# Optimization experiments

Measured on AMD Instinct MI355X. Metric: run time of the kernel, lower is better.

## Reference

```python
import jax, jax.numpy as jnp
import numpy as np

B, W, S, D, H = 16, 128, 16, 768, 12
HD = D // H

def _ln(x, g, b):
    m = x.mean(-1, keepdims=True)
    v = ((x - m) ** 2).mean(-1, keepdims=True)
    return (x - m) / jnp.sqrt(v + 1e-5) * g + b

def _lin(x, w, b):
    return x @ w.T + b

def _rope(t):
    # t: (N, H, L, HD); interleaved even/odd rotation, base 10000
    inv = 1.0 / (10000.0 ** (jnp.arange(0, HD, 2, dtype=jnp.float32) / HD))
    fr = jnp.arange(t.shape[2], dtype=jnp.float32)[:, None] * inv[None, :]  # (L, HD//2)
    cos, sin = jnp.cos(fr), jnp.sin(fr)
    te, to = t[..., ::2], t[..., 1::2]
    return jnp.stack([te * cos - to * sin, te * sin + to * cos], -1).reshape(t.shape)

def _mha(q, k, v, mask=None):
    # q,k,v: (N, H, L, HD)
    s = jnp.einsum('nhqd,nhkd->nhqk', q, k) / jnp.sqrt(jnp.float32(HD))
    if mask is not None:
        s = jnp.where(mask[None, None], -jnp.inf, s)
    a = jax.nn.softmax(s, axis=-1)
    return jnp.einsum('nhqk,nhkd->nhqd', a, v)

def _heads(t, L):
    return t.reshape(-1, L, H, HD).transpose(0, 2, 1, 3)

def setup_inputs() -> dict:
    key = jax.random.key(0)
    ks = jax.random.split(key, 16)
    def w(i, shape):
        return jax.random.normal(ks[i], shape, jnp.float32) * 0.02
    return {
        'x': jax.random.normal(ks[0], (B, W, S, D), jnp.float32),
        'causal_mask': jnp.triu(jnp.ones((W, W), dtype=bool), k=1),
        'sn_g': jnp.ones((D,), jnp.float32), 'sn_b': jnp.zeros((D,), jnp.float32),
        'sa_in_w': w(1, (3 * D, D)), 'sa_in_b': jnp.zeros((3 * D,), jnp.float32),
        'sa_out_w': w(2, (D, D)), 'sa_out_b': jnp.zeros((D,), jnp.float32),
        'tn_g': jnp.ones((D,), jnp.float32), 'tn_b': jnp.zeros((D,), jnp.float32),
        'tq_w': w(3, (D, D)), 'tq_b': jnp.zeros((D,), jnp.float32),
        'tk_w': w(4, (D, D)), 'tk_b': jnp.zeros((D,), jnp.float32),
        'tv_w': w(5, (D, D)), 'tv_b': jnp.zeros((D,), jnp.float32),
        'to_w': w(6, (D, D)), 'to_b': jnp.zeros((D,), jnp.float32),
        'fn_g': jnp.ones((D,), jnp.float32), 'fn_b': jnp.zeros((D,), jnp.float32),
        'f1_w': w(7, (4 * D, D)), 'f1_b': jnp.zeros((4 * D,), jnp.float32),
        'f2_w': w(8, (D, 4 * D)), 'f2_b': jnp.zeros((D,), jnp.float32),
    }

def reference(x, causal_mask, sn_g, sn_b, sa_in_w, sa_in_b, sa_out_w, sa_out_b,
              tn_g, tn_b, tq_w, tq_b, tk_w, tk_b, tv_w, tv_b, to_w, to_b,
              fn_g, fn_b, f1_w, f1_b, f2_w, f2_b):
    # ---- spatial attention within each timestep: (B*W, S, D) ----
    xs = x.reshape(B * W, S, D)
    xn = _ln(xs, sn_g, sn_b)
    q, k, v = jnp.split(_lin(xn, sa_in_w, sa_in_b), 3, axis=-1)
    o = _mha(_heads(q, S), _heads(k, S), _heads(v, S))
    o = o.transpose(0, 2, 1, 3).reshape(B * W, S, D)
    xs = xs + _lin(o, sa_out_w, sa_out_b)
    x = xs.reshape(B, W, S, D)
    # ---- causal temporal attention with RoPE: (B*S, W, D) ----
    xt = x.transpose(0, 2, 1, 3).reshape(B * S, W, D)
    xn = _ln(xt, tn_g, tn_b)
    q = _rope(_heads(_lin(xn, tq_w, tq_b), W))
    k = _rope(_heads(_lin(xn, tk_w, tk_b), W))
    v = _heads(_lin(xn, tv_w, tv_b), W)
    o = _mha(q, k, v, causal_mask)
    o = o.transpose(0, 2, 1, 3).reshape(B * S, W, D)
    xt = xt + _lin(o, to_w, to_b)
    x = xt.reshape(B, S, W, D).transpose(0, 2, 1, 3)
    # ---- feed-forward (exact GELU, as torch default) ----
    h = jax.nn.gelu(_lin(_ln(x, fn_g, fn_b), f1_w, f1_b), approximate=False)
    return x + _lin(h, f2_w, f2_b)
```

## Files before the change

kernel.cpp:

```cpp
#include <hip/hip_runtime.h>
#include <stdint.h>


#define NB 16
#define NW 128
#define NS 16
#define ND 768
#define NH 12
#define NTOK 32768

typedef __attribute__((ext_vector_type(8))) short short8;
typedef __attribute__((ext_vector_type(4))) float f32x4;

__device__ __forceinline__ float blo(unsigned v){ return __builtin_bit_cast(float, v << 16); }
__device__ __forceinline__ float bhi(unsigned v){ return __builtin_bit_cast(float, v & 0xffff0000u); }
__device__ __forceinline__ float bus(unsigned short u){ return __builtin_bit_cast(float, ((unsigned)u) << 16); }
__device__ __forceinline__ unsigned short f2b(float f){
  unsigned u = __builtin_bit_cast(unsigned, f);
  u += 0x7fffu + ((u >> 16) & 1u);
  return (unsigned short)(u >> 16);
}
__device__ __forceinline__ void gld_lds16(const void* g, void* l){
  __builtin_amdgcn_global_load_lds((const __attribute__((address_space(1))) void*)g,
                                   (__attribute__((address_space(3))) void*)l, 16, 0, 0);
}

__global__ __launch_bounds__(256) void convert_k(const float* __restrict__ in,
                                                 unsigned short* __restrict__ out, int n4){
  int i = blockIdx.x * 256 + threadIdx.x;
  int stride = gridDim.x * 256;
  for (; i < n4; i += stride){
    float4 v = ((const float4*)in)[i];
    unsigned lo = (unsigned)f2b(v.x) | ((unsigned)f2b(v.y) << 16);
    unsigned hi = (unsigned)f2b(v.z) | ((unsigned)f2b(v.w) << 16);
    ((uint2*)out)[i] = make_uint2(lo, hi);
  }
}

__global__ __launch_bounds__(256) void concat3_k(const float* __restrict__ a, const float* __restrict__ b,
                                                 const float* __restrict__ c, float* __restrict__ o){
  int i = blockIdx.x * 256 + threadIdx.x;
  if (i < 768){ o[i] = a[i]; o[768 + i] = b[i]; o[1536 + i] = c[i]; }
}

__global__ __launch_bounds__(256) void rope_k(float* __restrict__ tab){
  int i = blockIdx.x * 256 + threadIdx.x;
  if (i < 128 * 32){
    int w = i >> 5, p = i & 31;
    float inv = powf(10000.0f, -((float)(2 * p)) / 64.0f);
    float ang = (float)w * inv;
    tab[i * 2] = cosf(ang);
    tab[i * 2 + 1] = sinf(ang);
  }
}

template<int INF32>
__global__ __launch_bounds__(256) void ln_k(const void* __restrict__ xin, const float* __restrict__ g,
                                            const float* __restrict__ bt, unsigned short* __restrict__ out){
  const int row = blockIdx.x;
  const int t = threadIdx.x;
  const float* xf = (const float*)xin;
  const unsigned short* xb = (const unsigned short*)xin;
  float v[3];
#pragma unroll
  for (int i = 0; i < 3; ++i){
    int j = t + i * 256;
    v[i] = INF32 ? xf[(size_t)row * 768 + j] : bus(xb[(size_t)row * 768 + j]);
  }
  float s = v[0] + v[1] + v[2];
  float ss = v[0]*v[0] + v[1]*v[1] + v[2]*v[2];
#pragma unroll
  for (int o = 1; o < 64; o <<= 1){ s += __shfl_xor(s, o, 64); ss += __shfl_xor(ss, o, 64); }
  __shared__ float red[8];
  int w = t >> 6;
  if ((t & 63) == 0){ red[w*2] = s; red[w*2+1] = ss; }
  __syncthreads();
  s = red[0] + red[2] + red[4] + red[6];
  ss = red[1] + red[3] + red[5] + red[7];
  float mean = s * (1.0f / 768.0f);
  float var = ss * (1.0f / 768.0f) - mean * mean;
  float rstd = rsqrtf(var + 1e-5f);
#pragma unroll
  for (int i = 0; i < 3; ++i){
    int j = t + i * 256;
    out[(size_t)row * 768 + j] = f2b((v[i] - mean) * rstd * g[j] + bt[j]);
  }
}

template<int MODE, int MROWS>
__global__ __launch_bounds__(512) void gemm256_k(const unsigned short* __restrict__ A,
                                                 const unsigned short* __restrict__ Bw,
                                                 const float* __restrict__ bias,
                                                 const void* __restrict__ resid,
                                                 void* __restrict__ outp, int K, int M){
  constexpr int MH = MROWS / 2;
  constexpr int ASH = (MROWS == 8) ? 14 : 13;
  constexpr int NJA = MROWS / 4;
  constexpr int LDSZ = 4 * (1 << ASH) + 65536;
  __shared__ char LB[LDSZ];
  char* const Asl = LB;
  char* const Bsl = LB + 4 * (1 << ASH);
  const int tid = threadIdx.x;
  const int lane = tid & 63, w = tid >> 6;
  const int llo = lane & 15, lhi = lane >> 4;
  const int wm = w >> 2, wn = w & 3;
  const int NT = K >> 6;

  const int gx = gridDim.x;
  const int nwg = gx * gridDim.y;
  const int orig = blockIdx.y * gx + blockIdx.x;
  const int lin = (nwg & 7) ? orig : ((orig & 7) * (nwg >> 3) + (orig >> 3));
  const int by = lin / gx, bx = lin - by * gx;
  const int brow = by * (MROWS << 5);
  const int bcol = bx << 8;

  const int r0 = tid >> 3, cp = tid & 7;
  const int swz = (cp << 4) ^ ((r0 & 7) << 4);
  const char* aG = (const char*)(A + (size_t)(brow + r0) * K) + swz;
  const char* bG = (const char*)(Bw + (size_t)(bcol + r0) * K) + swz;
  const int J  = K * 128;
  const int Ha = K * (MROWS << 5);
  const int Hb = K * 256;
  const int ldst = w << 10;

  auto stage_a = [&](int gb, char* slotbase){
    gld_lds16(aG + gb, slotbase + ldst);
    if constexpr (NJA == 2) gld_lds16(aG + gb + J, slotbase + ldst + (1 << 13));
  };
  auto stage_b = [&](int gb, char* slotbase){
    gld_lds16(bG + gb, slotbase + ldst);
    gld_lds16(bG + gb + J, slotbase + ldst + (1 << 13));
  };

  short8 a0[MH][2], a1[MH][2], b0[2][2], b1[2][2];
  auto rd_a = [&](short8 (&dst)[MH][2], const char* Ab, int rbase){
#pragma unroll
    for (int mi = 0; mi < MH; ++mi){
      const int rr = rbase + (mi << 4) + llo;
#pragma unroll
      for (int ks = 0; ks < 2; ++ks)
        dst[mi][ks] = *(const short8*)(Ab + rr * 128 + (((ks << 6) + (lhi << 4)) ^ ((rr & 7) << 4)));
    }
  };
  auto rd_b = [&](short8 (&dst)[2][2], const char* Bb, int cbase){
#pragma unroll
    for (int ni = 0; ni < 2; ++ni){
      const int cc = cbase + (ni << 4) + llo;
#pragma unroll
      for (int ks = 0; ks < 2; ++ks)
        dst[ni][ks] = *(const short8*)(Bb + cc * 128 + (((ks << 6) + (lhi << 4)) ^ ((cc & 7) << 4)));
    }
  };

  f32x4 acc[MROWS][4];
#pragma unroll
  for (int m = 0; m < MROWS; ++m)
#pragma unroll
    for (int n = 0; n < 4; ++n) acc[m][n] = f32x4{0.f, 0.f, 0.f, 0.f};

  auto mfma_q = [&](int mo, int no, short8 (&bb)[2][2], short8 (&aa)[MH][2]){
    __builtin_amdgcn_s_setprio(1);
#pragma unroll
    for (int mi = 0; mi < MH; ++mi)
#pragma unroll
      for (int ni = 0; ni < 2; ++ni){
        acc[mo + mi][no + ni] = __builtin_amdgcn_mfma_f32_16x16x32_bf16(bb[ni][0], aa[mi][0], acc[mo + mi][no + ni], 0, 0, 0);
        acc[mo + mi][no + ni] = __builtin_amdgcn_mfma_f32_16x16x32_bf16(bb[ni][1], aa[mi][1], acc[mo + mi][no + ni], 0, 0, 0);
      }
    __builtin_amdgcn_s_setprio(0);
  };

  stage_a(0,        Asl);
  stage_a(Ha,       Asl + (1 << ASH));
  stage_b(0,        Bsl);
  stage_b(Hb,       Bsl + (1 << 14));
  stage_a(128,      Asl + (2 << ASH));
  stage_a(128 + Ha, Asl + (3 << ASH));
  if constexpr (NJA == 2) asm volatile("s_waitcnt vmcnt(4)" ::: "memory");
  else                    asm volatile("s_waitcnt vmcnt(2)" ::: "memory");
  __builtin_amdgcn_s_barrier();
  {
    const char* Ab0 = Asl + ((wm & 3) << ASH);
    const char* Bb0 = Bsl + (((wn >> 1) & 3) << 14);
    rd_b(b0, Bb0, (wn & 1) << 6);
    rd_a(a0, Ab0, 0);
  }

  for (int t = 0; t < NT; ++t){
    const char* Ab = Asl + (((2 * t + wm) & 3) << ASH);
    const char* Bb = Bsl + (((2 * t + (wn >> 1)) & 3) << 14);
    const int tb = t << 7;

    rd_a(a1, Ab, MH << 4);
    __builtin_amdgcn_s_barrier();
    mfma_q(0, 0, b0, a0);
    __builtin_amdgcn_s_barrier();

    rd_b(b1, Bb, ((wn & 1) << 6) + 32);
    if (t + 1 < NT) stage_b(tb + 128, Bsl + (((2 * t + 2) & 3) << 14));
    __builtin_amdgcn_s_barrier();
    mfma_q(MH, 0, b0, a1);
    __builtin_amdgcn_s_barrier();

    if (t + 1 < NT) stage_b(tb + 128 + Hb, Bsl + (((2 * t + 3) & 3) << 14));
    if (t + 2 < NT) stage_a(tb + 256, Asl + (((2 * t + 4) & 3) << ASH));
    __builtin_amdgcn_s_barrier();
    mfma_q(0, 2, b1, a0);
    __builtin_amdgcn_s_barrier();

    if (t + 2 < NT){
      stage_a(tb + 256 + Ha, Asl + (((2 * t + 5) & 3) << ASH));
      if constexpr (NJA == 2) asm volatile("s_waitcnt vmcnt(4)" ::: "memory");
      else                    asm volatile("s_waitcnt vmcnt(2)" ::: "memory");
    } else {
      asm volatile("s_waitcnt vmcnt(0)" ::: "memory");
    }
    __builtin_amdgcn_s_barrier();
    if (t + 1 < NT){
      const char* Abn = Asl + (((2 * t + 2 + wm) & 3) << ASH);
      const char* Bbn = Bsl + (((2 * t + 2 + (wn >> 1)) & 3) << 14);
      rd_b(b0, Bbn, (wn & 1) << 6);
      rd_a(a0, Abn, 0);
    }
    mfma_q(MH, 2, b1, a1);
    __builtin_amdgcn_s_barrier();
  }

  const int orow = brow + wm * (MROWS << 4);
  const int ocol = bcol + (wn << 6);
  const unsigned short* resb = (const unsigned short*)resid;
  const float* resf = (const float*)resid;
#pragma unroll
  for (int m = 0; m < MROWS; ++m){
    const int row = orow + (m << 4) + llo;
    const size_t rb = (size_t)row * M;
#pragma unroll
    for (int n = 0; n < 4; ++n){
      const int col = ocol + (n << 4) + (lhi << 2);
      const float4 bv = *(const float4*)&bias[col];
      float v0 = acc[m][n][0] + bv.x;
      float v1 = acc[m][n][1] + bv.y;
      float v2 = acc[m][n][2] + bv.z;
      float v3 = acc[m][n][3] + bv.w;
      const size_t off = rb + col;
      if (MODE == 1){
        float y0 = v0 * (1.5957691216f + 0.0713548163f * v0 * v0);
        float y1 = v1 * (1.5957691216f + 0.0713548163f * v1 * v1);
        float y2 = v2 * (1.5957691216f + 0.0713548163f * v2 * v2);
        float y3 = v3 * (1.5957691216f + 0.0713548163f * v3 * v3);
        v0 = v0 / (1.0f + __expf(-y0));
        v1 = v1 / (1.0f + __expf(-y1));
        v2 = v2 / (1.0f + __expf(-y2));
        v3 = v3 / (1.0f + __expf(-y3));
      } else if (MODE == 2){
        const float4 rv = *(const float4*)&resf[off];
        v0 += rv.x; v1 += rv.y; v2 += rv.z; v3 += rv.w;
      } else if (MODE == 3 || MODE == 4){
        const uint2 rv = *(const uint2*)&resb[off];
        v0 += blo(rv.x); v1 += bhi(rv.x); v2 += blo(rv.y); v3 += bhi(rv.y);
      }
      if (MODE == 4){
        float4 ov; ov.x = v0; ov.y = v1; ov.z = v2; ov.w = v3;
        *(float4*)&((float*)outp)[off] = ov;
      } else {
        unsigned lo = (unsigned)f2b(v0) | ((unsigned)f2b(v1) << 16);
        unsigned hi = (unsigned)f2b(v2) | ((unsigned)f2b(v3) << 16);
        *(uint2*)&((unsigned short*)outp)[off] = make_uint2(lo, hi);
      }
    }
  }
}

__global__ __launch_bounds__(256) void sattn_k(const unsigned short* __restrict__ qkv,
                                               unsigned short* __restrict__ o){
  const int bw = blockIdx.x, h = blockIdx.y;
  const int t = threadIdx.x;
  __shared__ unsigned short qh[16 * 68], kh[16 * 68], vh[16 * 68];
  __shared__ float pl[16 * 17];
  const int row = t >> 4, c4 = t & 15;
  const size_t base = ((size_t)(bw * 16 + row)) * 2304 + h * 64 + c4 * 4;
  *(uint2*)&qh[row * 68 + c4 * 4] = *(const uint2*)&qkv[base];
  *(uint2*)&kh[row * 68 + c4 * 4] = *(const uint2*)&qkv[base + 768];
  *(uint2*)&vh[row * 68 + c4 * 4] = *(const uint2*)&qkv[base + 1536];
  __syncthreads();

  const int q = row, k = c4;
  float s = 0.f;
#pragma unroll
  for (int c = 0; c < 16; ++c){
    uint2 qv = *(const uint2*)&qh[q * 68 + c * 4];
    uint2 kv = *(const uint2*)&kh[k * 68 + c * 4];
    s += blo(qv.x) * blo(kv.x) + bhi(qv.x) * bhi(kv.x);
    s += blo(qv.y) * blo(kv.y) + bhi(qv.y) * bhi(kv.y);
  }
  s *= 0.125f;
  float m = s;
#pragma unroll
  for (int off = 1; off < 16; off <<= 1) m = fmaxf(m, __shfl_xor(m, off, 64));
  float p = __expf(s - m);
  float su = p;
#pragma unroll
  for (int off = 1; off < 16; off <<= 1) su += __shfl_xor(su, off, 64);
  pl[q * 17 + k] = p / su;
  __syncthreads();

  float o0 = 0.f, o1 = 0.f, o2 = 0.f, o3 = 0.f;
#pragma unroll
  for (int kk = 0; kk < 16; ++kk){
    float pw = pl[q * 17 + kk];
    uint2 vv = *(const uint2*)&vh[kk * 68 + c4 * 4];
    o0 += pw * blo(vv.x); o1 += pw * bhi(vv.x);
    o2 += pw * blo(vv.y); o3 += pw * bhi(vv.y);
  }
  const size_t ob = ((size_t)(bw * 16 + q)) * 768 + h * 64 + c4 * 4;
  unsigned r0 = (unsigned)f2b(o0) | ((unsigned)f2b(o1) << 16);
  unsigned r1 = (unsigned)f2b(o2) | ((unsigned)f2b(o3) << 16);
  *(uint2*)&o[ob] = make_uint2(r0, r1);
}

__global__ __launch_bounds__(256) void tattn_k(const unsigned short* __restrict__ qkv,
                                               const float* __restrict__ rope,
                                               unsigned short* __restrict__ o){
  const int bs = blockIdx.x, h = blockIdx.y;
  const int b = bs >> 4, s = bs & 15;
  const int t = threadIdx.x, lane = t & 63, w = t >> 6;
  const int lhi = lane >> 4, llo = lane & 15;
  __shared__ unsigned short Qs[128 * 64];
  __shared__ unsigned short Ks[128 * 64];
  __shared__ unsigned short Vt[64 * 128];
  __shared__ unsigned short P[128 * 128];

  {
    const int r = t >> 1;
    const int dbase = (t & 1) * 32;
    const size_t tokb = ((size_t)((b * 128 + r) * 16 + s)) * 2304 + h * 64;
    const float2* rp = (const float2*)rope;
#pragma unroll
    for (int mch = 0; mch < 4; ++mch){
      const int d0 = dbase + mch * 8;
      uint4 qv = *(const uint4*)&qkv[tokb + d0];
      uint4 kv = *(const uint4*)&qkv[tokb + 768 + d0];
      uint4 vv = *(const uint4*)&qkv[tokb + 1536 + d0];
      unsigned qin[4] = {qv.x, qv.y, qv.z, qv.w};
      unsigned kin[4] = {kv.x, kv.y, kv.z, kv.w};
      unsigned qo[4], ko[4];
#pragma unroll
      for (int j = 0; j < 4; ++j){
        float2 cssn = rp[r * 32 + (d0 >> 1) + j];
        float cs = cssn.x, sn = cssn.y;
        float qe = blo(qin[j]), qd = bhi(qin[j]);
        float ke = blo(kin[j]), kd = bhi(kin[j]);
        qo[j] = (unsigned)f2b(qe * cs - qd * sn) | ((unsigned)f2b(qe * sn + qd * cs) << 16);
        ko[j] = (unsigned)f2b(ke * cs - kd * sn) | ((unsigned)f2b(ke * sn + kd * cs) << 16);
      }
      const int byq = r * 128 + ((d0 * 2) ^ ((r & 7) << 4));
      *(uint4*)((char*)Qs + byq) = make_uint4(qo[0], qo[1], qo[2], qo[3]);
      *(uint4*)((char*)Ks + byq) = make_uint4(ko[0], ko[1], ko[2], ko[3]);
      unsigned vin[4] = {vv.x, vv.y, vv.z, vv.w};
#pragma unroll
      for (int j = 0; j < 8; ++j){
        const int d = d0 + j;
        unsigned short val = (j & 1) ? (unsigned short)(vin[j >> 1] >> 16)
                                     : (unsigned short)(vin[j >> 1] & 0xffffu);
        *(unsigned short*)((char*)Vt + d * 256 + ((r * 2) ^ ((d & 7) << 4))) = val;
      }
    }
  }
  __syncthreads();

  const int qbase = w * 32;
  f32x4 st[8][2];
#pragma unroll
  for (int i = 0; i < 8; ++i){ st[i][0] = f32x4{0.f,0.f,0.f,0.f}; st[i][1] = f32x4{0.f,0.f,0.f,0.f}; }
#pragma unroll
  for (int kd = 0; kd < 2; ++kd){
    short8 bq[2];
#pragma unroll
    for (int fq = 0; fq < 2; ++fq){
      const int qr = qbase + fq * 16 + llo;
      bq[fq] = *(const short8*)((const char*)Qs + qr * 128 + ((kd * 64 + lhi * 16) ^ ((qr & 7) << 4)));
    }
#pragma unroll
    for (int fk = 0; fk < 8; ++fk){
      const int kr = fk * 16 + llo;
      short8 ak = *(const short8*)((const char*)Ks + kr * 128 + ((kd * 64 + lhi * 16) ^ ((kr & 7) << 4)));
      st[fk][0] = __builtin_amdgcn_mfma_f32_16x16x32_bf16(ak, bq[0], st[fk][0], 0, 0, 0);
      st[fk][1] = __builtin_amdgcn_mfma_f32_16x16x32_bf16(ak, bq[1], st[fk][1], 0, 0, 0);
    }
  }

#pragma unroll
  for (int fq = 0; fq < 2; ++fq){
    const int qg = qbase + fq * 16 + llo;
    float m = -1e30f;
#pragma unroll
    for (int fk = 0; fk < 8; ++fk)
#pragma unroll
      for (int rr = 0; rr < 4; ++rr){
        const int kg = fk * 16 + lhi * 4 + rr;
        float sv = (kg <= qg) ? st[fk][fq][rr] : -1e30f;
        st[fk][fq][rr] = sv;
        m = fmaxf(m, sv);
      }
    m = fmaxf(m, __shfl_xor(m, 16, 64));
    m = fmaxf(m, __shfl_xor(m, 32, 64));
    float su = 0.f;
#pragma unroll
    for (int fk = 0; fk < 8; ++fk)
#pragma unroll
      for (int rr = 0; rr < 4; ++rr){
        float p = __expf((st[fk][fq][rr] - m) * 0.125f);
        st[fk][fq][rr] = p;
        su += p;
      }
    su += __shfl_xor(su, 16, 64);
    su += __shfl_xor(su, 32, 64);
    const float rs = 1.0f / su;
#pragma unroll
    for (int fk = 0; fk < 8; ++fk){
      const int kk = fk * 16 + lhi * 4;
      unsigned lo = (unsigned)f2b(st[fk][fq][0] * rs) | ((unsigned)f2b(st[fk][fq][1] * rs) << 16);
      unsigned hi = (unsigned)f2b(st[fk][fq][2] * rs) | ((unsigned)f2b(st[fk][fq][3] * rs) << 16);
      *(uint2*)((char*)P + qg * 256 + ((kk * 2) ^ ((qg & 7) << 4))) = make_uint2(lo, hi);
    }
  }
  __syncthreads();

  f32x4 oacc[2][4];
#pragma unroll
  for (int i = 0; i < 2; ++i)
#pragma unroll
    for (int j = 0; j < 4; ++j) oacc[i][j] = f32x4{0.f,0.f,0.f,0.f};
#pragma unroll
  for (int ks = 0; ks < 4; ++ks){
    short8 pa[2];
#pragma unroll
    for (int fq = 0; fq < 2; ++fq){
      const int qr = qbase + fq * 16 + llo;
      pa[fq] = *(const short8*)((const char*)P + qr * 256 + ((ks * 64 + lhi * 16) ^ ((qr & 7) << 4)));
    }
#pragma unroll
    for (int fd = 0; fd < 4; ++fd){
      const int dr = fd * 16 + llo;
      short8 vb = *(const short8*)((const char*)Vt + dr * 256 + ((ks * 64 + lhi * 16) ^ ((dr & 7) << 4)));
      oacc[0][fd] = __builtin_amdgcn_mfma_f32_16x16x32_bf16(pa[0], vb, oacc[0][fd], 0, 0, 0);
      oacc[1][fd] = __builtin_amdgcn_mfma_f32_16x16x32_bf16(pa[1], vb, oacc[1][fd], 0, 0, 0);
    }
  }

#pragma unroll
  for (int fq = 0; fq < 2; ++fq)
#pragma unroll
    for (int fd = 0; fd < 4; ++fd)
#pragma unroll
      for (int rr = 0; rr < 4; ++rr){
        const int qg = qbase + fq * 16 + lhi * 4 + rr;
        const int d = fd * 16 + llo;
        const size_t ob = ((size_t)((b * 128 + qg) * 16 + s)) * 768 + h * 64 + d;
        o[ob] = f2b(oacc[fq][fd][rr]);
      }
}

__global__ __launch_bounds__(256) void sentinel_k(float* out){
  if (blockIdx.x == 0 && threadIdx.x == 0) out[0] = 12345.0f;
}

extern "C" void kernel_launch(void* const* d_in, const int* in_sizes, int n_in,
                              void* d_out, int out_size, void* d_ws, size_t ws_size,
                              hipStream_t stream){
  const float* x       = (const float*)d_in[0];
  const float* sn_g    = (const float*)d_in[2];
  const float* sn_b    = (const float*)d_in[3];
  const float* sa_in_w = (const float*)d_in[4];
  const float* sa_in_b = (const float*)d_in[5];
  const float* sa_out_w= (const float*)d_in[6];
  const float* sa_out_b= (const float*)d_in[7];
  const float* tn_g    = (const float*)d_in[8];
  const float* tn_b    = (const float*)d_in[9];
  const float* tq_w    = (const float*)d_in[10];
  const float* tq_b    = (const float*)d_in[11];
  const float* tk_w    = (const float*)d_in[12];
  const float* tk_b    = (const float*)d_in[13];
  const float* tv_w    = (const float*)d_in[14];
  const float* tv_b    = (const float*)d_in[15];
  const float* to_w    = (const float*)d_in[16];
  const float* to_b    = (const float*)d_in[17];
  const float* fn_g    = (const float*)d_in[18];
  const float* fn_b    = (const float*)d_in[19];
  const float* f1_w    = (const float*)d_in[20];
  const float* f1_b    = (const float*)d_in[21];
  const float* f2_w    = (const float*)d_in[22];
  const float* f2_b    = (const float*)d_in[23];

  char* ws = (char*)d_ws;
  size_t off = 0;
  auto alloc = [&](size_t bytes) -> void* {
    void* p = ws + off;
    off += (bytes + 255) & ~(size_t)255;
    return p;
  };
  unsigned short* Wqkv = (unsigned short*)alloc((size_t)2304*768*2);
  unsigned short* Wo1  = (unsigned short*)alloc((size_t)768*768*2);
  unsigned short* W3   = (unsigned short*)alloc((size_t)2304*768*2);
  float*          b3   = (float*)alloc(2304*4);
  unsigned short* Wto  = (unsigned short*)alloc((size_t)768*768*2);
  unsigned short* Wf1  = (unsigned short*)alloc((size_t)3072*768*2);
  unsigned short* Wf2  = (unsigned short*)alloc((size_t)768*3072*2);
  float*          rope = (float*)alloc(128*32*2*4);
  unsigned short* xn   = (unsigned short*)alloc((size_t)NTOK*768*2);
  unsigned short* qkv  = (unsigned short*)alloc((size_t)NTOK*3072*2);
  unsigned short* xs2  = (unsigned short*)alloc((size_t)NTOK*768*2);
  unsigned short* xt2  = (unsigned short*)alloc((size_t)NTOK*768*2);
  unsigned short* ob   = xn;

  if (ws_size < off){ sentinel_k<<<1, 64, 0, stream>>>((float*)d_out); return; }

  convert_k<<<1024, 256, 0, stream>>>(sa_in_w, Wqkv, 2304*768/4);
  convert_k<<<512, 256, 0, stream>>>(sa_out_w, Wo1, 768*768/4);
  convert_k<<<512, 256, 0, stream>>>(tq_w, W3, 768*768/4);
  convert_k<<<512, 256, 0, stream>>>(tk_w, W3 + 768*768, 768*768/4);
  convert_k<<<512, 256, 0, stream>>>(tv_w, W3 + 2*768*768, 768*768/4);
  concat3_k<<<3, 256, 0, stream>>>(tq_b, tk_b, tv_b, b3);
  convert_k<<<512, 256, 0, stream>>>(to_w, Wto, 768*768/4);
  convert_k<<<1024, 256, 0, stream>>>(f1_w, Wf1, 3072*768/4);
  convert_k<<<1024, 256, 0, stream>>>(f2_w, Wf2, 768*3072/4);
  rope_k<<<16, 256, 0, stream>>>(rope);

  ln_k<1><<<NTOK, 256, 0, stream>>>(x, sn_g, sn_b, xn);
  gemm256_k<0,4><<<dim3(9, 256), 512, 0, stream>>>(xn, Wqkv, sa_in_b, nullptr, qkv, 768, 2304);
  sattn_k<<<dim3(2048, 12), 256, 0, stream>>>(qkv, ob);
  gemm256_k<2,4><<<dim3(3, 256), 512, 0, stream>>>(ob, Wo1, sa_out_b, x, xs2, 768, 768);

  ln_k<0><<<NTOK, 256, 0, stream>>>(xs2, tn_g, tn_b, xn);
  gemm256_k<0,4><<<dim3(9, 256), 512, 0, stream>>>(xn, W3, b3, nullptr, qkv, 768, 2304);
  tattn_k<<<dim3(256, 12), 256, 0, stream>>>(qkv, rope, ob);
  gemm256_k<3,4><<<dim3(3, 256), 512, 0, stream>>>(ob, Wto, to_b, xs2, xt2, 768, 768);

  ln_k<0><<<NTOK, 256, 0, stream>>>(xt2, fn_g, fn_b, xn);
  gemm256_k<1,8><<<dim3(12, 128), 512, 0, stream>>>(xn, Wf1, f1_b, nullptr, qkv, 768, 3072);
  gemm256_k<4,4><<<dim3(3, 256), 512, 0, stream>>>(qkv, Wf2, f2_b, xt2, d_out, 3072, 768);
}
```

Baseline: 1.176 ms.

## Replace 256-wide 8-wave GEMM with 128x128 4-wave tile at two blocks per CU

The large 512-thread GEMM, with a 128x256 or 256x256 output tile and 96-128KB of LDS, is replaced by a 256-thread kernel that computes a 128x128 tile and uses 64KB of LDS. Its launch bounds request two blocks per CU. The software pipeline is restructured: fragments are now read from LDS at each quarter-step, guarded by explicit lgkmcnt waits, instead of being prefetched across the barrier. The aim is higher occupancy and more blocks for load balance, at the cost of lower arithmetic intensity per tile, more global/L2 traffic, and more exposed LDS latency.

```diff
diff --git a/kernel.cpp b/kernel.cpp
--- a/kernel.cpp
+++ b/kernel.cpp
@@ -87,23 +87,19 @@
   }
 }
 
-template<int MODE, int MROWS>
-__global__ __launch_bounds__(512) void gemm256_k(const unsigned short* __restrict__ A,
-                                                 const unsigned short* __restrict__ Bw,
-                                                 const float* __restrict__ bias,
-                                                 const void* __restrict__ resid,
-                                                 void* __restrict__ outp, int K, int M){
-  constexpr int MH = MROWS / 2;
-  constexpr int ASH = (MROWS == 8) ? 14 : 13;
-  constexpr int NJA = MROWS / 4;
-  constexpr int LDSZ = 4 * (1 << ASH) + 65536;
-  __shared__ char LB[LDSZ];
+template<int MODE>
+__global__ __launch_bounds__(256, 2) void gemm128_k(const unsigned short* __restrict__ A,
+                                                    const unsigned short* __restrict__ Bw,
+                                                    const float* __restrict__ bias,
+                                                    const void* __restrict__ resid,
+                                                    void* __restrict__ outp, int K, int M){
+  __shared__ char LB[65536];
   char* const Asl = LB;
-  char* const Bsl = LB + 4 * (1 << ASH);
+  char* const Bsl = LB + 32768;
   const int tid = threadIdx.x;
   const int lane = tid & 63, w = tid >> 6;
   const int llo = lane & 15, lhi = lane >> 4;
-  const int wm = w >> 2, wn = w & 3;
+  const int wm = w >> 1, wn = w & 1;
   const int NT = K >> 6;
 
   const int gx = gridDim.x;
@@ -111,31 +107,26 @@
   const int orig = blockIdx.y * gx + blockIdx.x;
   const int lin = (nwg & 7) ? orig : ((orig & 7) * (nwg >> 3) + (orig >> 3));
   const int by = lin / gx, bx = lin - by * gx;
-  const int brow = by * (MROWS << 5);
-  const int bcol = bx << 8;
+  const int brow = by << 7;
+  const int bcol = bx << 7;
 
   const int r0 = tid >> 3, cp = tid & 7;
   const int swz = (cp << 4) ^ ((r0 & 7) << 4);
   const char* aG = (const char*)(A + (size_t)(brow + r0) * K) + swz;
   const char* bG = (const char*)(Bw + (size_t)(bcol + r0) * K) + swz;
-  const int J  = K * 128;
-  const int Ha = K * (MROWS << 5);
-  const int Hb = K * 256;
+  const int J  = K * 64;
+  const int Hh = K * 128;
   const int ldst = w << 10;
 
-  auto stage_a = [&](int gb, char* slotbase){
-    gld_lds16(aG + gb, slotbase + ldst);
-    if constexpr (NJA == 2) gld_lds16(aG + gb + J, slotbase + ldst + (1 << 13));
+  auto stage = [&](const char* g, int gb, char* slotbase){
+    gld_lds16(g + gb,     slotbase + ldst);
+    gld_lds16(g + gb + J, slotbase + ldst + (1 << 12));
   };
-  auto stage_b = [&](int gb, char* slotbase){
-    gld_lds16(bG + gb, slotbase + ldst);
-    gld_lds16(bG + gb + J, slotbase + ldst + (1 << 13));
-  };
-
-  short8 a0[MH][2], a1[MH][2], b0[2][2], b1[2][2];
-  auto rd_a = [&](short8 (&dst)[MH][2], const char* Ab, int rbase){
-#pragma unroll
-    for (int mi = 0; mi < MH; ++mi){
+
+  short8 a0[2][2], a1[2][2], b0[2][2], b1[2][2];
+  auto rd_a = [&](short8 (&dst)[2][2], const char* Ab, int rbase){
+#pragma unroll
+    for (int mi = 0; mi < 2; ++mi){
       const int rr = rbase + (mi << 4) + llo;
 #pragma unroll
       for (int ks = 0; ks < 2; ++ks)
@@ -152,16 +143,16 @@
     }
   };
 
-  f32x4 acc[MROWS][4];
-#pragma unroll
-  for (int m = 0; m < MROWS; ++m)
+  f32x4 acc[4][4];
+#pragma unroll
+  for (int m = 0; m < 4; ++m)
 #pragma unroll
     for (int n = 0; n < 4; ++n) acc[m][n] = f32x4{0.f, 0.f, 0.f, 0.f};
 
-  auto mfma_q = [&](int mo, int no, short8 (&bb)[2][2], short8 (&aa)[MH][2]){
+  auto mfma_q = [&](int mo, int no, short8 (&bb)[2][2], short8 (&aa)[2][2]){
     __builtin_amdgcn_s_setprio(1);
 #pragma unroll
-    for (int mi = 0; mi < MH; ++mi)
+    for (int mi = 0; mi < 2; ++mi)
 #pragma unroll
       for (int ni = 0; ni < 2; ++ni){
         acc[mo + mi][no + ni] = __builtin_amdgcn_mfma_f32_16x16x32_bf16(bb[ni][0], aa[mi][0], acc[mo + mi][no + ni], 0, 0, 0);
@@ -170,68 +161,57 @@
     __builtin_amdgcn_s_setprio(0);
   };
 
-  stage_a(0,        Asl);
-  stage_a(Ha,       Asl + (1 << ASH));
-  stage_b(0,        Bsl);
-  stage_b(Hb,       Bsl + (1 << 14));
-  stage_a(128,      Asl + (2 << ASH));
-  stage_a(128 + Ha, Asl + (3 << ASH));
-  if constexpr (NJA == 2) asm volatile("s_waitcnt vmcnt(4)" ::: "memory");
-  else                    asm volatile("s_waitcnt vmcnt(2)" ::: "memory");
+  stage(aG, 0,        Asl);
+  stage(aG, Hh,       Asl + (1 << 13));
+  stage(bG, 0,        Bsl);
+  stage(bG, Hh,       Bsl + (1 << 13));
+  stage(aG, 128,      Asl + (2 << 13));
+  stage(aG, 128 + Hh, Asl + (3 << 13));
+  asm volatile("s_waitcnt vmcnt(4)" ::: "memory");
   __builtin_amdgcn_s_barrier();
-  {
-    const char* Ab0 = Asl + ((wm & 3) << ASH);
-    const char* Bb0 = Bsl + (((wn >> 1) & 3) << 14);
-    rd_b(b0, Bb0, (wn & 1) << 6);
-    rd_a(a0, Ab0, 0);
-  }
 
   for (int t = 0; t < NT; ++t){
-    const char* Ab = Asl + (((2 * t + wm) & 3) << ASH);
-    const char* Bb = Bsl + (((2 * t + (wn >> 1)) & 3) << 14);
+    const char* Ab = Asl + (((2 * t + wm) & 3) << 13);
+    const char* Bb = Bsl + (((2 * t + wn) & 3) << 13);
     const int tb = t << 7;
 
-    rd_a(a1, Ab, MH << 4);
-    __builtin_amdgcn_s_barrier();
+    rd_b(b0, Bb, 0);
+    rd_a(a0, Ab, 0);
+    if (t + 1 < NT) stage(bG, tb + 128, Bsl + (((2 * t + 2) & 3) << 13));
+    __builtin_amdgcn_s_barrier();
+    asm volatile("s_waitcnt lgkmcnt(0)" ::: "memory");
     mfma_q(0, 0, b0, a0);
     __builtin_amdgcn_s_barrier();
 
-    rd_b(b1, Bb, ((wn & 1) << 6) + 32);
-    if (t + 1 < NT) stage_b(tb + 128, Bsl + (((2 * t + 2) & 3) << 14));
-    __builtin_amdgcn_s_barrier();
-    mfma_q(MH, 0, b0, a1);
-    __builtin_amdgcn_s_barrier();
-
-    if (t + 1 < NT) stage_b(tb + 128 + Hb, Bsl + (((2 * t + 3) & 3) << 14));
-    if (t + 2 < NT) stage_a(tb + 256, Asl + (((2 * t + 4) & 3) << ASH));
-    __builtin_amdgcn_s_barrier();
+    rd_a(a1, Ab, 32);
+    if (t + 1 < NT) stage(bG, tb + 128 + Hh, Bsl + (((2 * t + 3) & 3) << 13));
+    __builtin_amdgcn_s_barrier();
+    asm volatile("s_waitcnt lgkmcnt(0)" ::: "memory");
+    mfma_q(2, 0, b0, a1);
+    __builtin_amdgcn_s_barrier();
+
+    rd_b(b1, Bb, 32);
+    if (t + 2 < NT) stage(aG, tb + 256, Asl + (((2 * t + 4) & 3) << 13));
+    __builtin_amdgcn_s_barrier();
+    asm volatile("s_waitcnt lgkmcnt(0)" ::: "memory");
     mfma_q(0, 2, b1, a0);
     __builtin_amdgcn_s_barrier();
 
-    if (t + 2 < NT){
-      stage_a(tb + 256 + Ha, Asl + (((2 * t + 5) & 3) << ASH));
-      if constexpr (NJA == 2) asm volatile("s_waitcnt vmcnt(4)" ::: "memory");
-      else                    asm volatile("s_waitcnt vmcnt(2)" ::: "memory");
-    } else {
-      asm volatile("s_waitcnt vmcnt(0)" ::: "memory");
-    }
-    __builtin_amdgcn_s_barrier();
-    if (t + 1 < NT){
-      const char* Abn = Asl + (((2 * t + 2 + wm) & 3) << ASH);
-      const char* Bbn = Bsl + (((2 * t + 2 + (wn >> 1)) & 3) << 14);
-      rd_b(b0, Bbn, (wn & 1) << 6);
-      rd_a(a0, Abn, 0);
-    }
-    mfma_q(MH, 2, b1, a1);
-    __builtin_amdgcn_s_barrier();
-  }
-
-  const int orow = brow + wm * (MROWS << 4);
+    if (t + 2 < NT) stage(aG, tb + 256 + Hh, Asl + (((2 * t + 5) & 3) << 13));
+    __builtin_amdgcn_s_barrier();
+    asm volatile("s_waitcnt lgkmcnt(0)" ::: "memory");
+    mfma_q(2, 2, b1, a1);
+    if (t + 2 < NT) asm volatile("s_waitcnt vmcnt(4)" ::: "memory");
+    else            asm volatile("s_waitcnt vmcnt(0)" ::: "memory");
+    __builtin_amdgcn_s_barrier();
+  }
+
+  const int orow = brow + (wm << 6);
   const int ocol = bcol + (wn << 6);
   const unsigned short* resb = (const unsigned short*)resid;
   const float* resf = (const float*)resid;
 #pragma unroll
-  for (int m = 0; m < MROWS; ++m){
+  for (int m = 0; m < 4; ++m){
     const int row = orow + (m << 4) + llo;
     const size_t rb = (size_t)row * M;
 #pragma unroll
@@ -527,16 +507,16 @@
   rope_k<<<16, 256, 0, stream>>>(rope);
 
   ln_k<1><<<NTOK, 256, 0, stream>>>(x, sn_g, sn_b, xn);
-  gemm256_k<0,4><<<dim3(9, 256), 512, 0, stream>>>(xn, Wqkv, sa_in_b, nullptr, qkv, 768, 2304);
+  gemm128_k<0><<<dim3(18, 256), 256, 0, stream>>>(xn, Wqkv, sa_in_b, nullptr, qkv, 768, 2304);
   sattn_k<<<dim3(2048, 12), 256, 0, stream>>>(qkv, ob);
-  gemm256_k<2,4><<<dim3(3, 256), 512, 0, stream>>>(ob, Wo1, sa_out_b, x, xs2, 768, 768);
+  gemm128_k<2><<<dim3(6, 256), 256, 0, stream>>>(ob, Wo1, sa_out_b, x, xs2, 768, 768);
 
   ln_k<0><<<NTOK, 256, 0, stream>>>(xs2, tn_g, tn_b, xn);
-  gemm256_k<0,4><<<dim3(9, 256), 512, 0, stream>>>(xn, W3, b3, nullptr, qkv, 768, 2304);
+  gemm128_k<0><<<dim3(18, 256), 256, 0, stream>>>(xn, W3, b3, nullptr, qkv, 768, 2304);
   tattn_k<<<dim3(256, 12), 256, 0, stream>>>(qkv, rope, ob);
-  gemm256_k<3,4><<<dim3(3, 256), 512, 0, stream>>>(ob, Wto, to_b, xs2, xt2, 768, 768);
+  gemm128_k<3><<<dim3(6, 256), 256, 0, stream>>>(ob, Wto, to_b, xs2, xt2, 768, 768);
 
   ln_k<0><<<NTOK, 256, 0, stream>>>(xt2, fn_g, fn_b, xn);
-  gemm256_k<1,8><<<dim3(12, 128), 512, 0, stream>>>(xn, Wf1, f1_b, nullptr, qkv, 768, 3072);
-  gemm256_k<4,4><<<dim3(3, 256), 512, 0, stream>>>(qkv, Wf2, f2_b, xt2, d_out, 3072, 768);
-}
+  gemm128_k<1><<<dim3(24, 256), 256, 0, stream>>>(xn, Wf1, f1_b, nullptr, qkv, 768, 3072);
+  gemm128_k<4><<<dim3(6, 256), 256, 0, stream>>>(qkv, Wf2, f2_b, xt2, d_out, 3072, 768);
+}
```

Result: faster. 1.106 ms (-5.9%).
